# Optimization experiments

Measured on AMD Instinct MI355X. Metric: run time of the kernel, lower is better.

## Reference

```python
import jax, jax.numpy as jnp
import numpy as np

D = 256   # input_size
H = 512   # hidden_size
A = 4     # alpha_dim
K = 2 * A * A  # output values per input dim (binary=False -> 2 params)


def _masks():
    # MADE sequential-ordering masks, per DART.create_masks
    in_deg = np.arange(D)
    hid_deg = np.arange(H) % (D - 1)
    out_deg = np.arange(D) - 1  # arange(D) % D - 1
    m0 = (hid_deg[:, None] >= in_deg[None, :]).astype(np.float32)   # [H, D]
    mh = (hid_deg[:, None] >= hid_deg[None, :]).astype(np.float32)  # [H, H]
    ml = (out_deg[:, None] >= hid_deg[None, :]).astype(np.float32)  # [D, H]
    # repeat(1, K).view(-1, H): each output-dim row repeated K consecutive times
    ml = np.repeat(ml, K, axis=0)                                    # [D*K, H]
    return jnp.asarray(m0), jnp.asarray(mh), jnp.asarray(ml)


def setup_inputs() -> dict:
    key = jax.random.key(0)
    ks = jax.random.split(key, 10)
    B = 1024
    x = jax.random.normal(ks[0], (B, D), dtype=jnp.float32)
    def lin(k, out_dim, in_dim):
        s = 1.0 / np.sqrt(in_dim)
        kw, kb = jax.random.split(k)
        W = jax.random.uniform(kw, (out_dim, in_dim), jnp.float32, -s, s)
        b = jax.random.uniform(kb, (out_dim,), jnp.float32, -s, s)
        return W, b
    W0, b0 = lin(ks[1], H, D)
    W1, b1 = lin(ks[2], H, H)
    W2, b2 = lin(ks[3], H, H)
    Wout, bout = lin(ks[4], D * K, H)
    # unnormalized_log_p_alpha initialized to log(1/A)
    ulpa = jnp.full((1, D - 1, 1, A), -np.log(A), dtype=jnp.float32)
    return {"x": x, "W0": W0, "b0": b0, "W1": W1, "b1": b1,
            "W2": W2, "b2": b2, "Wout": Wout, "bout": bout, "ulpa": ulpa}


def reference(x, W0, b0, W1, b1, W2, b2, Wout, bout, ulpa):
    m0, mh, ml = _masks()
    B = x.shape[0]
    # masked MLP (MADE)
    h = jax.nn.relu(x @ (m0 * W0).T + b0)
    h = jax.nn.relu(h @ (mh * W1).T + b1)
    h = jax.nn.relu(h @ (mh * W2).T + b2)
    theta = (h @ (ml * Wout).T + bout).reshape(B, D, 2, A, A)
    mu = theta[:, :, 0]                      # [B, D, A, A]
    std = jnp.exp(theta[:, :, 1]) + 0.01     # [B, D, A, A]
    xe = x[:, :, None, None]
    # Normal log-prob
    log_px = -0.5 * jnp.square((xe - mu) / std) - jnp.log(std) - 0.5 * jnp.log(2.0 * jnp.pi)
    # normalized log p(alpha): [1, D-1, 1, A]
    lpa = jax.nn.log_softmax(ulpa, axis=-1)
    joint = log_px[:, :-1] + lpa             # [B, D-1, A, A]
    first = joint[:, 0, 0:1]                 # [B, 1, A]
    inner = jnp.swapaxes(joint[:, 1:], 0, 1)  # [D-2, B, A, A]
    # HMM-style forward recursion: stable log-domain chain matmul via scan
    def step(carry, m):
        # carry: [B, 1, A]; m: [B, A, A]
        new = jax.nn.logsumexp(carry[:, :, :, None] + m[:, None, :, :], axis=-2)
        return new, None
    carry, _ = jax.lax.scan(step, first, inner)
    last = log_px[:, -1, :, 0:1]             # [B, A, 1]
    log_p = jax.nn.logsumexp(carry[:, :, :, None] + last[:, None, :, :], axis=-2)  # [B,1,1]
    return log_p, theta
```

## Files before the change

### kernel.cpp

```cpp
#include <hip/hip_runtime.h>
#include <math.h>

#define Bsz 1024
#define Dd  256
#define Hh  512
#define NOUT 8192

typedef __attribute__((ext_vector_type(8))) short bf8_t;
typedef __attribute__((ext_vector_type(4))) float f4_t;

__device__ inline ushort f2b(float f) {
  union { float f; unsigned u; } c; c.f = f;
  unsigned r = c.u + 0x7fffu + ((c.u >> 16) & 1u);
  return (ushort)(r >> 16);
}

__device__ inline void async16(const ushort* g, ushort* l) {
  __builtin_amdgcn_global_load_lds((const __attribute__((address_space(1))) void*)g,
                                   (__attribute__((address_space(3))) void*)l, 16, 0, 0);
}

__device__ inline int mod255(int v) {
  if (v >= 510) return v - 510;
  if (v >= 255) return v - 255;
  return v;
}

__global__ __launch_bounds__(256) void prep(
    const float* __restrict__ x,  const float* __restrict__ W0,
    const float* __restrict__ W1, const float* __restrict__ W2,
    const float* __restrict__ Wout, const float* __restrict__ ulpa,
    ushort* __restrict__ xb, ushort* __restrict__ w0b, ushort* __restrict__ w1b,
    ushort* __restrict__ w2b, ushort* __restrict__ woutb,
    float* __restrict__ lpa)
{
  const int blk = blockIdx.x, tid = threadIdx.x;
  if (blk == 2496) {
    if (tid < Dd - 1) {
      float v0 = ulpa[tid * 4 + 0], v1 = ulpa[tid * 4 + 1];
      float v2 = ulpa[tid * 4 + 2], v3 = ulpa[tid * 4 + 3];
      float m = fmaxf(fmaxf(v0, v1), fmaxf(v2, v3));
      float s = __expf(v0 - m) + __expf(v1 - m) + __expf(v2 - m) + __expf(v3 - m);
      float l = m + __logf(s);
      lpa[tid * 4 + 0] = v0 - l;
      lpa[tid * 4 + 1] = v1 - l;
      lpa[tid * 4 + 2] = v2 - l;
      lpa[tid * 4 + 3] = v3 - l;
    }
    return;
  }
  const float* src; ushort* dst; int lb, mode;
  if (blk < 128)      { src = x;    dst = xb;    lb = blk;       mode = 0; }
  else if (blk < 192) { src = W0;   dst = w0b;   lb = blk - 128; mode = 1; }
  else if (blk < 320) { src = W1;   dst = w1b;   lb = blk - 192; mode = 2; }
  else if (blk < 448) { src = W2;   dst = w2b;   lb = blk - 320; mode = 2; }
  else                { src = Wout; dst = woutb; lb = blk - 448; mode = 3; }

  const int e = lb * 2048 + tid * 8;
  float4 v0 = *(const float4*)(src + e);
  float4 v1 = *(const float4*)(src + e + 4);
  float vv[8] = {v0.x, v0.y, v0.z, v0.w, v1.x, v1.y, v1.z, v1.w};
  ushort u[8];
  if (mode == 0) {
#pragma unroll
    for (int i = 0; i < 8; i++) u[i] = f2b(vv[i]);
  } else if (mode == 1) {
    int n = e >> 8, k0 = e & 255, nd = mod255(n);
#pragma unroll
    for (int i = 0; i < 8; i++) u[i] = (nd >= k0 + i) ? f2b(vv[i]) : (ushort)0;
  } else if (mode == 2) {
    int n = e >> 9, k0 = e & 511, nd = mod255(n);
#pragma unroll
    for (int i = 0; i < 8; i++) u[i] = (nd >= mod255(k0 + i)) ? f2b(vv[i]) : (ushort)0;
  } else {
    int n = e >> 9, k0 = e & 511, nd = (n >> 5) - 1;
#pragma unroll
    for (int i = 0; i < 8; i++) u[i] = (nd >= mod255(k0 + i)) ? f2b(vv[i]) : (ushort)0;
  }
  *(ushort4*)(dst + e)     = *(ushort4*)&u[0];
  *(ushort4*)(dst + e + 4) = *(ushort4*)&u[4];
}

template<int KD>
__global__ __launch_bounds__(256) void gemm_s(
    const ushort* __restrict__ A, const ushort* __restrict__ W,
    const float* __restrict__ bias, ushort* __restrict__ Ch)
{
  __shared__ ushort As[64 * 64];
  __shared__ ushort Bs[32 * 64];
  const int tid = threadIdx.x, lane = tid & 63, wave = tid >> 6;
  const int row0 = blockIdx.y * 64, col0 = blockIdx.x * 32;
  const int fm = lane & 15, qq = lane >> 4;
  const int srow = lane >> 3, qslot = lane & 7;

  f4_t acc[2];
  acc[0] = (f4_t){0.f, 0.f, 0.f, 0.f};
  acc[1] = (f4_t){0.f, 0.f, 0.f, 0.f};

  for (int kt = 0; kt < KD; kt += 64) {
#pragma unroll
    for (int a = 0; a < 2; a++) {
      int rb = wave * 16 + a * 8;
      int r = rb + srow;
      int q = (qslot - r) & 7;
      async16(A + (size_t)(row0 + r) * KD + kt + q * 8, &As[rb * 64]);
    }
    {
      int rb = wave * 8;
      int r = rb + srow;
      int q = (qslot - r) & 7;
      async16(W + (size_t)(col0 + r) * KD + kt + q * 8, &Bs[rb * 64]);
    }
    __syncthreads();
#pragma unroll
    for (int t = 0; t < 2; t++) {
      int ra = wave * 16 + fm;
      int slota = ((t * 4 + qq) + ra) & 7;
      bf8_t af = *(const bf8_t*)&As[ra * 64 + slota * 8];
#pragma unroll
      for (int j = 0; j < 2; j++) {
        int rb = j * 16 + fm;
        int slot = ((t * 4 + qq) + rb) & 7;
        bf8_t bf = *(const bf8_t*)&Bs[rb * 64 + slot * 8];
        acc[j] = __builtin_amdgcn_mfma_f32_16x16x32_bf16(af, bf, acc[j], 0, 0, 0);
      }
    }
    __syncthreads();
  }

#pragma unroll
  for (int j = 0; j < 2; j++) {
    int col = col0 + j * 16 + fm;
    float bv = bias[col];
    int rbase = row0 + wave * 16 + qq * 4;
#pragma unroll
    for (int r = 0; r < 4; r++) {
      float t = fmaxf(acc[j][r] + bv, 0.0f);
      Ch[(size_t)(rbase + r) * Hh + col] = f2b(t);
    }
  }
}

__global__ __launch_bounds__(256) void gemm_big(
    const ushort* __restrict__ A, const ushort* __restrict__ W,
    const float* __restrict__ bias, float* __restrict__ Cf,
    int M, int N, int Kd)
{
  __shared__ ushort As[128 * 64];
  __shared__ ushort Bs[128 * 64];
  const int tid = threadIdx.x, lane = tid & 63, wave = tid >> 6;
  const int waveM = wave >> 1, waveN = wave & 1;
  const int row0 = blockIdx.y * 128, col0 = blockIdx.x * 128;
  const int fm = lane & 15, qq = lane >> 4;
  const int srow = lane >> 3, qslot = lane & 7;

  f4_t acc[4][4];
#pragma unroll
  for (int i = 0; i < 4; i++)
#pragma unroll
    for (int j = 0; j < 4; j++) acc[i][j] = (f4_t){0.f, 0.f, 0.f, 0.f};

  for (int kt = 0; kt < Kd; kt += 64) {
#pragma unroll
    for (int p = 0; p < 4; p++) {
      int rb = p * 32 + wave * 8;
      int r = rb + srow;
      int q = (qslot - r) & 7;
      async16(A + (size_t)(row0 + r) * Kd + kt + q * 8, &As[rb * 64]);
    }
#pragma unroll
    for (int p = 0; p < 4; p++) {
      int rb = p * 32 + wave * 8;
      int r = rb + srow;
      int q = (qslot - r) & 7;
      async16(W + (size_t)(col0 + r) * Kd + kt + q * 8, &Bs[rb * 64]);
    }
    __syncthreads();
#pragma unroll
    for (int t = 0; t < 2; t++) {
      bf8_t af[4], bf[4];
#pragma unroll
      for (int i = 0; i < 4; i++) {
        int r = waveM * 64 + i * 16 + fm;
        int slot = ((t * 4 + qq) + r) & 7;
        af[i] = *(const bf8_t*)&As[r * 64 + slot * 8];
      }
#pragma unroll
      for (int j = 0; j < 4; j++) {
        int r = waveN * 64 + j * 16 + fm;
        int slot = ((t * 4 + qq) + r) & 7;
        bf[j] = *(const bf8_t*)&Bs[r * 64 + slot * 8];
      }
#pragma unroll
      for (int i = 0; i < 4; i++)
#pragma unroll
        for (int j = 0; j < 4; j++)
          acc[i][j] = __builtin_amdgcn_mfma_f32_16x16x32_bf16(af[i], bf[j], acc[i][j], 0, 0, 0);
    }
    __syncthreads();
  }

#pragma unroll
  for (int j = 0; j < 4; j++) {
    int col = col0 + waveN * 64 + j * 16 + fm;
    float bv = bias[col];
#pragma unroll
    for (int i = 0; i < 4; i++) {
      int rbase = row0 + waveM * 64 + i * 16 + qq * 4;
#pragma unroll
      for (int r = 0; r < 4; r++)
        Cf[(size_t)(rbase + r) * N + col] = acc[i][j][r] + bv;
    }
  }
}

__global__ __launch_bounds__(256) void chain2(
    const float* __restrict__ x, const float* __restrict__ theta,
    const float* __restrict__ lpa, float* __restrict__ logp)
{
  const int b = blockIdx.x;
  const int tid = threadIdx.x;
  const int seg = tid >> 4, e = tid & 15;
  const int i = e >> 2, jj = e & 3;
  const int base = (tid & 63) & ~15;
  const float C0 = 0.91893853320467274178f;
  const float* th = theta + (size_t)b * NOUT;
  const float* xb = x + (size_t)b * Dd;
  __shared__ float Ts[16][16];

  const int d0 = 1 + seg * 16;
  const int d1 = min(d0 + 16, Dd - 1);

  auto stepm = [&](int d) -> float {
    float mu = th[d * 32 + e];
    float ls = th[d * 32 + 16 + e];
    float s  = __expf(ls) + 0.01f;
    float z  = (xb[d] - mu) * __builtin_amdgcn_rcpf(s);
    return -0.5f * z * z - __logf(s) - C0 + lpa[d * 4 + jj];
  };

  float T = stepm(d0);
  for (int d = d0 + 1; d < d1; d++) {
    float m_ = stepm(d);
    float v0 = __shfl(T, base + i * 4 + 0) + __shfl(m_, base + 0 * 4 + jj);
    float v1 = __shfl(T, base + i * 4 + 1) + __shfl(m_, base + 1 * 4 + jj);
    float v2 = __shfl(T, base + i * 4 + 2) + __shfl(m_, base + 2 * 4 + jj);
    float v3 = __shfl(T, base + i * 4 + 3) + __shfl(m_, base + 3 * 4 + jj);
    float mx = fmaxf(fmaxf(v0, v1), fmaxf(v2, v3));
    float s  = __expf(v0 - mx) + __expf(v1 - mx) + __expf(v2 - mx) + __expf(v3 - mx);
    T = mx + __logf(s);
  }
  Ts[seg][e] = T;
  __syncthreads();

  if (tid < 4) {
    const int j = tid;
    float mu = th[j], ls = th[16 + j];
    float s = __expf(ls) + 0.01f;
    float z = (xb[0] - mu) * __builtin_amdgcn_rcpf(s);
    float carry = -0.5f * z * z - __logf(s) - C0 + lpa[j];
#pragma unroll 1
    for (int sg = 0; sg < 16; sg++) {
      float c0 = __shfl(carry, 0);
      float c1 = __shfl(carry, 1);
      float c2 = __shfl(carry, 2);
      float c3 = __shfl(carry, 3);
      float v0 = c0 + Ts[sg][0 * 4 + j];
      float v1 = c1 + Ts[sg][1 * 4 + j];
      float v2 = c2 + Ts[sg][2 * 4 + j];
      float v3 = c3 + Ts[sg][3 * 4 + j];
      float mx = fmaxf(fmaxf(v0, v1), fmaxf(v2, v3));
      float ss = __expf(v0 - mx) + __expf(v1 - mx) + __expf(v2 - mx) + __expf(v3 - mx);
      carry = mx + __logf(ss);
    }
    float mu2 = th[255 * 32 + j * 4], ls2 = th[255 * 32 + 16 + j * 4];
    float s2 = __expf(ls2) + 0.01f;
    float z2 = (xb[255] - mu2) * __builtin_amdgcn_rcpf(s2);
    float v = carry - 0.5f * z2 * z2 - __logf(s2) - C0;
    float mx = fmaxf(v, __shfl_xor(v, 1));
    mx = fmaxf(mx, __shfl_xor(mx, 2));
    float ee = __expf(v - mx);
    ee += __shfl_xor(ee, 1);
    ee += __shfl_xor(ee, 2);
    if (j == 0) logp[b] = mx + __logf(ee);
  }
}

extern "C" void kernel_launch(void* const* d_in, const int* in_sizes, int n_in,
                              void* d_out, int out_size, void* d_ws, size_t ws_size,
                              hipStream_t stream)
{
  const float* x    = (const float*)d_in[0];
  const float* W0   = (const float*)d_in[1];
  const float* b0   = (const float*)d_in[2];
  const float* W1   = (const float*)d_in[3];
  const float* b1   = (const float*)d_in[4];
  const float* W2   = (const float*)d_in[5];
  const float* b2   = (const float*)d_in[6];
  const float* Wout = (const float*)d_in[7];
  const float* bout = (const float*)d_in[8];
  const float* ulpa = (const float*)d_in[9];

  float* out   = (float*)d_out;
  float* logp  = out;
  float* theta = out + Bsz;

  ushort* ws    = (ushort*)d_ws;
  ushort* xb    = ws;
  ushort* w0b   = xb + 262144;
  ushort* w1b   = w0b + 131072;
  ushort* w2b   = w1b + 262144;
  ushort* woutb = w2b + 262144;
  ushort* h0    = woutb + 4194304;
  ushort* h1    = h0 + 524288;
  ushort* h2    = h1 + 524288;
  float*  lpa   = (float*)(h2 + 524288);

  prep<<<2497, 256, 0, stream>>>(x, W0, W1, W2, Wout, ulpa,
                                 xb, w0b, w1b, w2b, woutb, lpa);
  gemm_s<Dd><<<dim3(16, 16), 256, 0, stream>>>(xb, w0b, b0, h0);
  gemm_s<Hh><<<dim3(16, 16), 256, 0, stream>>>(h0, w1b, b1, h1);
  gemm_s<Hh><<<dim3(16, 16), 256, 0, stream>>>(h1, w2b, b2, h2);
  gemm_big<<<dim3(NOUT / 128, Bsz / 128), 256, 0, stream>>>(h2, woutb, bout, theta, Bsz, NOUT, Hh);
  chain2<<<Bsz, 256, 0, stream>>>(x, theta, lpa, logp);
}
```

Baseline: 138.0 us.

## Fuse HMM segment products into output GEMM epilogue and add fold kernel

After: 193.6 us. 40.2% more time.

```diff
diff --git a/kernel.cpp b/kernel.cpp
--- a/kernel.cpp
+++ b/kernel.cpp
@@ -5,6 +5,7 @@
 #define Dd  256
 #define Hh  512
 #define NOUT 8192
+#define C0f 0.91893853320467274178f
 
 typedef __attribute__((ext_vector_type(8))) short bf8_t;
 typedef __attribute__((ext_vector_type(4))) float f4_t;
@@ -144,15 +145,19 @@
 __global__ __launch_bounds__(256) void gemm_big(
     const ushort* __restrict__ A, const ushort* __restrict__ W,
     const float* __restrict__ bias, float* __restrict__ Cf,
-    int M, int N, int Kd)
+    const float* __restrict__ x, const float* __restrict__ lpa,
+    float* __restrict__ Tseg)
 {
   __shared__ ushort As[128 * 64];
   __shared__ ushort Bs[128 * 64];
+  __shared__ float Ct[32][133];
   const int tid = threadIdx.x, lane = tid & 63, wave = tid >> 6;
   const int waveM = wave >> 1, waveN = wave & 1;
-  const int row0 = blockIdx.y * 128, col0 = blockIdx.x * 128;
+  const int bx = blockIdx.x;
+  const int row0 = blockIdx.y * 128, col0 = bx * 128;
   const int fm = lane & 15, qq = lane >> 4;
   const int srow = lane >> 3, qslot = lane & 7;
+  const int Kd = Hh, N = NOUT;
 
   f4_t acc[4][4];
 #pragma unroll
@@ -212,78 +217,98 @@
         Cf[(size_t)(rbase + r) * N + col] = acc[i][j][r] + bv;
     }
   }
-}
-
-__global__ __launch_bounds__(256) void chain2(
-    const float* __restrict__ x, const float* __restrict__ theta,
-    const float* __restrict__ lpa, float* __restrict__ logp)
-{
-  const int b = blockIdx.x;
+
+  for (int ch = 0; ch < 4; ch++) {
+    __syncthreads();
+    if (waveM == (ch >> 1)) {
+      int ibase = (ch & 1) * 2;
+#pragma unroll
+      for (int ii = 0; ii < 2; ii++) {
+        int i = ibase + ii;
+        int crow = i * 16 + qq * 4 - (ch & 1) * 32;
+#pragma unroll
+        for (int j = 0; j < 4; j++) {
+          int ccol = waveN * 64 + j * 16 + fm;
+          float bv = bias[col0 + ccol];
+#pragma unroll
+          for (int r = 0; r < 4; r++)
+            Ct[crow + r][ccol] = acc[i][j][r] + bv;
+        }
+      }
+    }
+    __syncthreads();
+    if (tid < 128) {
+      const int bl = tid >> 2, dl = tid & 3;
+      const int b = row0 + ch * 32 + bl;
+      const int d = 4 * bx + dl;
+      const float xv = x[b * Dd + d];
+      float lp[4] = {0.f, 0.f, 0.f, 0.f};
+      if (d < 255) {
+        lp[0] = lpa[d * 4 + 0]; lp[1] = lpa[d * 4 + 1];
+        lp[2] = lpa[d * 4 + 2]; lp[3] = lpa[d * 4 + 3];
+      }
+      float M[16];
+#pragma unroll
+      for (int e = 0; e < 16; e++) {
+        int src = (d == 0) ? (e & 3) : (d == 255 ? (e & 12) : e);
+        float mu = Ct[bl][dl * 32 + src];
+        float ls = Ct[bl][dl * 32 + 16 + src];
+        float s  = __expf(ls) + 0.01f;
+        float z  = (xv - mu) * __builtin_amdgcn_rcpf(s);
+        float v  = -0.5f * z * z - __logf(s) - C0f;
+        if (d < 255) v += lp[e & 3];
+        M[e] = v;
+      }
+      const int l = tid & 63;
+      const int pe = l & ~1, pb = l & ~3;
+      float P[16];
+#pragma unroll
+      for (int e = 0; e < 16; e++) {
+        int i = e >> 2, j = e & 3;
+        float a0 = __shfl(M[i * 4 + 0], pe) + __shfl(M[0 * 4 + j], pe | 1);
+        float a1 = __shfl(M[i * 4 + 1], pe) + __shfl(M[1 * 4 + j], pe | 1);
+        float a2 = __shfl(M[i * 4 + 2], pe) + __shfl(M[2 * 4 + j], pe | 1);
+        float a3 = __shfl(M[i * 4 + 3], pe) + __shfl(M[3 * 4 + j], pe | 1);
+        float mx = fmaxf(fmaxf(a0, a1), fmaxf(a2, a3));
+        P[e] = mx + __logf(__expf(a0 - mx) + __expf(a1 - mx) + __expf(a2 - mx) + __expf(a3 - mx));
+      }
+      float T[16];
+#pragma unroll
+      for (int e = 0; e < 16; e++) {
+        int i = e >> 2, j = e & 3;
+        float a0 = __shfl(P[i * 4 + 0], pb) + __shfl(P[0 * 4 + j], pb | 2);
+        float a1 = __shfl(P[i * 4 + 1], pb) + __shfl(P[1 * 4 + j], pb | 2);
+        float a2 = __shfl(P[i * 4 + 2], pb) + __shfl(P[2 * 4 + j], pb | 2);
+        float a3 = __shfl(P[i * 4 + 3], pb) + __shfl(P[3 * 4 + j], pb | 2);
+        float mx = fmaxf(fmaxf(a0, a1), fmaxf(a2, a3));
+        T[e] = mx + __logf(__expf(a0 - mx) + __expf(a1 - mx) + __expf(a2 - mx) + __expf(a3 - mx));
+      }
+      float4 tq = {T[dl * 4 + 0], T[dl * 4 + 1], T[dl * 4 + 2], T[dl * 4 + 3]};
+      *(float4*)&Tseg[((size_t)b * 64 + bx) * 16 + dl * 4] = tq;
+    }
+  }
+}
+
+__global__ __launch_bounds__(256) void foldk(
+    const float* __restrict__ Tseg, float* __restrict__ logp)
+{
   const int tid = threadIdx.x;
-  const int seg = tid >> 4, e = tid & 15;
-  const int i = e >> 2, jj = e & 3;
-  const int base = (tid & 63) & ~15;
-  const float C0 = 0.91893853320467274178f;
-  const float* th = theta + (size_t)b * NOUT;
-  const float* xb = x + (size_t)b * Dd;
-  __shared__ float Ts[16][16];
-
-  const int d0 = 1 + seg * 16;
-  const int d1 = min(d0 + 16, Dd - 1);
-
-  auto stepm = [&](int d) -> float {
-    float mu = th[d * 32 + e];
-    float ls = th[d * 32 + 16 + e];
-    float s  = __expf(ls) + 0.01f;
-    float z  = (xb[d] - mu) * __builtin_amdgcn_rcpf(s);
-    return -0.5f * z * z - __logf(s) - C0 + lpa[d * 4 + jj];
-  };
-
-  float T = stepm(d0);
-  for (int d = d0 + 1; d < d1; d++) {
-    float m_ = stepm(d);
-    float v0 = __shfl(T, base + i * 4 + 0) + __shfl(m_, base + 0 * 4 + jj);
-    float v1 = __shfl(T, base + i * 4 + 1) + __shfl(m_, base + 1 * 4 + jj);
-    float v2 = __shfl(T, base + i * 4 + 2) + __shfl(m_, base + 2 * 4 + jj);
-    float v3 = __shfl(T, base + i * 4 + 3) + __shfl(m_, base + 3 * 4 + jj);
-    float mx = fmaxf(fmaxf(v0, v1), fmaxf(v2, v3));
-    float s  = __expf(v0 - mx) + __expf(v1 - mx) + __expf(v2 - mx) + __expf(v3 - mx);
-    T = mx + __logf(s);
-  }
-  Ts[seg][e] = T;
-  __syncthreads();
-
-  if (tid < 4) {
-    const int j = tid;
-    float mu = th[j], ls = th[16 + j];
-    float s = __expf(ls) + 0.01f;
-    float z = (xb[0] - mu) * __builtin_amdgcn_rcpf(s);
-    float carry = -0.5f * z * z - __logf(s) - C0 + lpa[j];
-#pragma unroll 1
-    for (int sg = 0; sg < 16; sg++) {
-      float c0 = __shfl(carry, 0);
-      float c1 = __shfl(carry, 1);
-      float c2 = __shfl(carry, 2);
-      float c3 = __shfl(carry, 3);
-      float v0 = c0 + Ts[sg][0 * 4 + j];
-      float v1 = c1 + Ts[sg][1 * 4 + j];
-      float v2 = c2 + Ts[sg][2 * 4 + j];
-      float v3 = c3 + Ts[sg][3 * 4 + j];
-      float mx = fmaxf(fmaxf(v0, v1), fmaxf(v2, v3));
-      float ss = __expf(v0 - mx) + __expf(v1 - mx) + __expf(v2 - mx) + __expf(v3 - mx);
-      carry = mx + __logf(ss);
-    }
-    float mu2 = th[255 * 32 + j * 4], ls2 = th[255 * 32 + 16 + j * 4];
-    float s2 = __expf(ls2) + 0.01f;
-    float z2 = (xb[255] - mu2) * __builtin_amdgcn_rcpf(s2);
-    float v = carry - 0.5f * z2 * z2 - __logf(s2) - C0;
-    float mx = fmaxf(v, __shfl_xor(v, 1));
-    mx = fmaxf(mx, __shfl_xor(mx, 2));
-    float ee = __expf(v - mx);
-    ee += __shfl_xor(ee, 1);
-    ee += __shfl_xor(ee, 2);
-    if (j == 0) logp[b] = mx + __logf(ee);
-  }
+  const int bl = tid >> 4, e = tid & 15;
+  const int b = blockIdx.x * 16 + bl;
+  const int l = tid & 63, base = l & ~15;
+  const int i = e >> 2, j = e & 3;
+  float C = Tseg[((size_t)b * 64 + 0) * 16 + e];
+#pragma unroll 4
+  for (int sg = 1; sg < 64; sg++) {
+    float T = Tseg[((size_t)b * 64 + sg) * 16 + e];
+    float a0 = __shfl(C, base + i * 4 + 0) + __shfl(T, base + 0 * 4 + j);
+    float a1 = __shfl(C, base + i * 4 + 1) + __shfl(T, base + 1 * 4 + j);
+    float a2 = __shfl(C, base + i * 4 + 2) + __shfl(T, base + 2 * 4 + j);
+    float a3 = __shfl(C, base + i * 4 + 3) + __shfl(T, base + 3 * 4 + j);
+    float mx = fmaxf(fmaxf(a0, a1), fmaxf(a2, a3));
+    C = mx + __logf(__expf(a0 - mx) + __expf(a1 - mx) + __expf(a2 - mx) + __expf(a3 - mx));
+  }
+  if (e == 0) logp[b] = C;
 }
 
 extern "C" void kernel_launch(void* const* d_in, const int* in_sizes, int n_in,
@@ -315,12 +340,13 @@
   ushort* h1    = h0 + 524288;
   ushort* h2    = h1 + 524288;
   float*  lpa   = (float*)(h2 + 524288);
+  float*  TsegW = lpa + 1024;
 
   prep<<<2497, 256, 0, stream>>>(x, W0, W1, W2, Wout, ulpa,
                                  xb, w0b, w1b, w2b, woutb, lpa);
   gemm_s<Dd><<<dim3(16, 16), 256, 0, stream>>>(xb, w0b, b0, h0);
   gemm_s<Hh><<<dim3(16, 16), 256, 0, stream>>>(h0, w1b, b1, h1);
   gemm_s<Hh><<<dim3(16, 16), 256, 0, stream>>>(h1, w2b, b2, h2);
-  gemm_big<<<dim3(NOUT / 128, Bsz / 128), 256, 0, stream>>>(h2, woutb, bout, theta, Bsz, NOUT, Hh);
-  chain2<<<Bsz, 256, 0, stream>>>(x, theta, lpa, logp);
-}
+  gemm_big<<<dim3(NOUT / 128, Bsz / 128), 256, 0, stream>>>(h2, woutb, bout, theta, x, lpa, TsegW);
+  foldk<<<Bsz / 16, 256, 0, stream>>>(TsegW, logp);
+}
```
